# Kernel optimization log

Measured on AMD Instinct MI355X. Metric: run time of the kernel, lower is better.

Reference implementation:

```python
import jax, jax.numpy as jnp
from jax import lax
import numpy as np

H = 512  # hidden_size

def lstm_cell(x, h, c, w_ih, w_hh):
    # gates: [B, 4H], pytorch LSTMCell gate order i, f, g, o
    gates = x @ w_ih.T + h @ w_hh.T
    i, f, g, o = jnp.split(gates, 4, axis=-1)
    c_new = jax.nn.sigmoid(f) * c + jax.nn.sigmoid(i) * jnp.tanh(g)
    h_new = jax.nn.sigmoid(o) * jnp.tanh(c_new)
    return h_new, c_new

def run_layer(xs, w_ih, w_hh):
    # xs: [T, B, D] -> hs, cs: [T, B, H]
    B = xs.shape[1]
    h0 = jnp.zeros((B, H), xs.dtype)
    c0 = jnp.zeros((B, H), xs.dtype)
    def step(carry, x):
        h, c = carry
        h, c = lstm_cell(x, h, c, w_ih, w_hh)
        return (h, c), (h, c)
    _, (hs, cs) = lax.scan(step, (h0, c0), xs)
    return hs, cs

def stacked(x, weights, reverse):
    # Faithful to apex stackedRNN: for reverse pass, the returned hidden
    # (collect_hidden=False) is the state after the FIRST reversed step
    # (seq == seq_len-1), per the `elif seq == seq_len - 1` branch.
    xs = x[::-1] if reverse else x
    h_hid, c_hid = [], []
    cur = xs
    for w_ih, w_hh in weights:
        hs, cs = run_layer(cur, w_ih, w_hh)
        cur = hs
        idx = 0 if reverse else -1
        h_hid.append(hs[idx])
        c_hid.append(cs[idx])
    out = cur[::-1] if reverse else cur
    return out, jnp.stack(h_hid), jnp.stack(c_hid)

def setup_inputs() -> dict:
    key = jax.random.key(0)
    ks = jax.random.split(key, 9)
    T, B, D = 1024, 64, 512
    stdev = 1.0 / np.sqrt(H)
    d = {"x": jax.random.normal(ks[0], (T, B, D), dtype=jnp.float32)}
    names = ["w_ih_f0", "w_hh_f0", "w_ih_f1", "w_hh_f1",
             "w_ih_b0", "w_hh_b0", "w_ih_b1", "w_hh_b1"]
    for i, n in enumerate(names):
        d[n] = jax.random.uniform(ks[i + 1], (4 * H, 512), dtype=jnp.float32,
                                  minval=-stdev, maxval=stdev)
    return d

def reference(x, w_ih_f0, w_hh_f0, w_ih_f1, w_hh_f1,
              w_ih_b0, w_hh_b0, w_ih_b1, w_hh_b1):
    fwd_out, fh, fc = stacked(x, [(w_ih_f0, w_hh_f0), (w_ih_f1, w_hh_f1)], False)
    bwd_out, bh, bc = stacked(x, [(w_ih_b0, w_hh_b0), (w_ih_b1, w_hh_b1)], True)
    output = jnp.concatenate([fwd_out, bwd_out], axis=-1)  # [T, B, 2H]
    h = jnp.concatenate([fh, bh], axis=-1)  # [nLayers, B, 2H]
    c = jnp.concatenate([fc, bc], axis=-1)  # [nLayers, B, 2H]
    return output, h, c
```

## Files before the change

### kernel.cpp

```cpp
#include <hip/hip_runtime.h>

typedef short  sh8  __attribute__((ext_vector_type(8)));
typedef float  f32x4 __attribute__((ext_vector_type(4)));
typedef ushort ush4 __attribute__((ext_vector_type(4)));

#define TS 1024
#define BB 64
#define HH 512

#define HOFF 67108864ull
#define HC_DELTA 131072ull

#define BAR_WORDS 2120

static __device__ __forceinline__ float sigm(float x){ return 1.f/(1.f+__expf(-x)); }
static __device__ __forceinline__ float tanh_(float x){ return 1.f - 2.f/(__expf(2.f*x)+1.f); }
static __device__ __forceinline__ ushort f2bf(float f){
  unsigned u = __float_as_uint(f);
  u += 0x7fffu + ((u>>16)&1u);
  return (ushort)(u>>16);
}

__global__ __launch_bounds__(256) void cvt_w(
    const float* __restrict__ p0, const float* __restrict__ p1,
    const float* __restrict__ p2, const float* __restrict__ p3,
    const float* __restrict__ p4, const float* __restrict__ p5,
    const float* __restrict__ p6, const float* __restrict__ p7,
    ushort* __restrict__ wb, unsigned* __restrict__ bar)
{
  if (blockIdx.x == 0){
    for (unsigned i = threadIdx.x; i < BAR_WORDS; i += 256) bar[i] = 0u;
  }
  const unsigned gid = blockIdx.x*256 + threadIdx.x;
  const unsigned m = gid >> 18;
  const unsigned o = gid & 0x3FFFFu;
  const float* src;
  switch(m){
    case 0: src=p0; break; case 1: src=p1; break; case 2: src=p2; break; case 3: src=p3; break;
    case 4: src=p4; break; case 5: src=p5; break; case 6: src=p6; break; default: src=p7; break;
  }
  float4 f = *(const float4*)(src + (size_t)o*4);
  ush4 r; r.x=f2bf(f.x); r.y=f2bf(f.y); r.z=f2bf(f.z); r.w=f2bf(f.w);
  *(ush4*)(wb + ((size_t)m<<20) + (size_t)o*4) = r;
}

__global__ __launch_bounds__(256) void cvt_x(
    const float* __restrict__ x, ushort* __restrict__ xb)
{
  const unsigned gid = blockIdx.x*256 + threadIdx.x;
  float4 f = *(const float4*)(x + (size_t)gid*4);
  ush4 r; r.x=f2bf(f.x); r.y=f2bf(f.y); r.z=f2bf(f.z); r.w=f2bf(f.w);
  *(ush4*)(xb + (size_t)gid*4) = r;
}

static __device__ __forceinline__ sh8 ld_cvt8(const float* p){
  float4 f0 = *(const float4*)p;
  float4 f1 = *(const float4*)(p+4);
  sh8 r;
  r[0]=(short)f2bf(f0.x); r[1]=(short)f2bf(f0.y); r[2]=(short)f2bf(f0.z); r[3]=(short)f2bf(f0.w);
  r[4]=(short)f2bf(f1.x); r[5]=(short)f2bf(f1.y); r[6]=(short)f2bf(f1.z); r[7]=(short)f2bf(f1.w);
  return r;
}

static __device__ __forceinline__ void pipe_barrier(unsigned* ctr, unsigned* abortf)
{
  __syncthreads();
  if (threadIdx.x == 0){
    if (__hip_atomic_load(abortf, __ATOMIC_RELAXED, __HIP_MEMORY_SCOPE_AGENT) == 0u){
      __hip_atomic_fetch_add(ctr, 1u, __ATOMIC_RELEASE, __HIP_MEMORY_SCOPE_AGENT);
      unsigned spins = 0;
      while (__hip_atomic_load(ctr, __ATOMIC_ACQUIRE, __HIP_MEMORY_SCOPE_AGENT) < 128u){
        __builtin_amdgcn_s_sleep(1);
        if (++spins > (1u<<22)){
          __hip_atomic_store(abortf, 1u, __ATOMIC_RELAXED, __HIP_MEMORY_SCOPE_AGENT);
          break;
        }
      }
    }
  }
  __syncthreads();
}

template<bool XBF>
__global__ __launch_bounds__(256, 1) void lstm_persist(
    const float* __restrict__ xf, const ushort* __restrict__ xb,
    const ushort* __restrict__ wb,
    float* __restrict__ out, ushort* __restrict__ h_ws, unsigned* __restrict__ bar)
{
  const int group = blockIdx.x >> 6;
  const int w     = blockIdx.x & 63;
  const int lane  = threadIdx.x & 63;
  const int wv    = threadIdx.x >> 6;
  const int n     = lane & 15;
  const int q     = lane >> 4;

  unsigned* ctrbase = bar + (size_t)(group & 1) * 1056;
  unsigned* abortf  = bar + 2112;

  int wbase;
  if      (group==0) wbase = 0;
  else if (group==1) wbase = 4;
  else if (group==2) wbase = 2;
  else               wbase = 6;
  const ushort* wih = wb + ((size_t)wbase<<20);
  const ushort* whh = wb + ((size_t)(wbase+1)<<20);

  const int r0 = ((n>>3)  )*512 + w*8 + (n&7);
  const int r1 = ((n>>3)+2)*512 + w*8 + (n&7);
  const int arow = wv*16 + n;
  const size_t aoff  = (size_t)arow*HH + q*8;
  const size_t b0off = (size_t)r0*HH + q*8;
  const size_t b1off = (size_t)r1*HH + q*8;

  sh8 wi0[16], wi1[16], wh0[16], wh1[16];
#pragma unroll
  for (int kk=0; kk<16; ++kk){
    wi0[kk] = *(const sh8*)(wih + b0off + (size_t)kk*32);
    wi1[kk] = *(const sh8*)(wih + b1off + (size_t)kk*32);
    wh0[kk] = *(const sh8*)(whh + b0off + (size_t)kk*32);
    wh1[kk] = *(const sh8*)(whh + b1off + (size_t)kk*32);
  }

  const bool low = (n < 8);
  const int  col = w*8 + (n&7);
  float c_reg[4] = {0.f,0.f,0.f,0.f};

  sh8 ax[16];
  if (group < 2){
    if constexpr (XBF){
      const ushort* p = xb + ((group==0) ? (size_t)0 : (size_t)(TS-1)*(BB*HH));
#pragma unroll
      for (int kk=0;kk<16;++kk) ax[kk] = *(const sh8*)(p + aoff + (size_t)kk*32);
    } else {
      const float* p = xf + ((group==0) ? (size_t)0 : (size_t)(TS-1)*(BB*HH));
#pragma unroll
      for (int kk=0;kk<16;++kk) ax[kk] = ld_cvt8(p + aoff + (size_t)kk*32);
    }
  }

  for (int s = 0; s <= TS; ++s){
    const bool active = (group < 2) ? (s < TS) : (s > 0);
    if (active){
      const int  step   = (group < 2) ? s : (s-1);
      const bool have_h = (step > 0);
      const ushort* hsrc = h_ws + ((size_t)group*2 + ((s-1)&1))*(BB*HH);

      if (group >= 2){
        const ushort* xsb = h_ws + ((size_t)(group-2)*2 + ((s-1)&1))*(BB*HH);
#pragma unroll
        for (int kk=0;kk<16;++kk) ax[kk] = *(const sh8*)(xsb + aoff + (size_t)kk*32);
      }

      f32x4 acc0 = {0.f,0.f,0.f,0.f};
      f32x4 acc1 = {0.f,0.f,0.f,0.f};
#pragma unroll
      for (int kk=0;kk<16;++kk){
        acc0 = __builtin_amdgcn_mfma_f32_16x16x32_bf16(ax[kk], wi0[kk], acc0, 0, 0, 0);
        acc1 = __builtin_amdgcn_mfma_f32_16x16x32_bf16(ax[kk], wi1[kk], acc1, 0, 0, 0);
      }
      if (have_h){
#pragma unroll
        for (int kk=0;kk<16;++kk){
          sh8 ah = *(const sh8*)(hsrc + aoff + (size_t)kk*32);
          acc0 = __builtin_amdgcn_mfma_f32_16x16x32_bf16(ah, wh0[kk], acc0, 0, 0, 0);
          acc1 = __builtin_amdgcn_mfma_f32_16x16x32_bf16(ah, wh1[kk], acc1, 0, 0, 0);
        }
      }

      ushort* hdst = h_ws + ((size_t)group*2 + (s&1))*(BB*HH);
#pragma unroll
      for (int r=0; r<4; ++r){
        float v0 = acc0[r], v1 = acc1[r];
        float p0 = __shfl_xor(v0, 8, 64);
        float p1 = __shfl_xor(v1, 8, 64);
        if (low){
          const int row = wv*16 + q*4 + r;
          const float iv=v0, fv=p0, gv=v1, ov=p1;
          float cn = sigm(fv)*c_reg[r] + sigm(iv)*tanh_(gv);
          float hn = sigm(ov)*tanh_(cn);
          c_reg[r] = cn;
          hdst[(size_t)row*HH + col] = f2bf(hn);

          if (group == 2){
            out[((size_t)(s-1)*BB + row)*1024 + col] = hn;
          } else if (group == 3){
            out[((size_t)(TS-s)*BB + row)*1024 + 512 + col] = hn;
          }

          bool cap = false; size_t hoff = 0;
          if      (group==0 && s==TS-1){ cap=true; hoff = HOFF + (size_t)row*1024 + col; }
          else if (group==1 && s==0)   { cap=true; hoff = HOFF + (size_t)row*1024 + 512 + col; }
          else if (group==2 && s==TS)  { cap=true; hoff = HOFF + (size_t)(BB+row)*1024 + col; }
          else if (group==3 && s==1)   { cap=true; hoff = HOFF + (size_t)(BB+row)*1024 + 512 + col; }
          if (cap){
            out[hoff] = hn;
            out[hoff + HC_DELTA] = cn;
          }
        }
      }
    }

    if (group < 2 && (s+1) < TS){
      if constexpr (XBF){
        const ushort* p = xb + ((group==0) ? (size_t)(s+1)*(BB*HH) : (size_t)(TS-2-s)*(BB*HH));
#pragma unroll
        for (int kk=0;kk<16;++kk) ax[kk] = *(const sh8*)(p + aoff + (size_t)kk*32);
      } else {
        const float* p = xf + ((group==0) ? (size_t)(s+1)*(BB*HH) : (size_t)(TS-2-s)*(BB*HH));
#pragma unroll
        for (int kk=0;kk<16;++kk) ax[kk] = ld_cvt8(p + aoff + (size_t)kk*32);
      }
    }

    if (s < TS) pipe_barrier(ctrbase + s, abortf);
  }
}

extern "C" void kernel_launch(void* const* d_in, const int* in_sizes, int n_in,
                              void* d_out, int out_size, void* d_ws, size_t ws_size,
                              hipStream_t stream)
{
  const float* x = (const float*)d_in[0];
  const float* W[8];
  for (int i = 0; i < 8; ++i) W[i] = (const float*)d_in[i+1];
  float* out = (float*)d_out;

  char* ws = (char*)d_ws;
  unsigned* bar  = (unsigned*)ws;
  ushort*   h_ws = (ushort*)(ws + 524288);
  ushort*   wb   = (ushort*)(ws + 1048576);
  ushort*   xb   = (ushort*)(ws + 1048576 + 16777216);
  const bool xbf = ws_size >= (1048576ull + 16777216ull + 67108864ull);

  cvt_w<<<dim3(8192), dim3(256), 0, stream>>>(W[0],W[1],W[2],W[3],W[4],W[5],W[6],W[7], wb, bar);
  if (xbf) cvt_x<<<dim3(32768), dim3(256), 0, stream>>>(x, xb);

  if (xbf)
    lstm_persist<true ><<<dim3(256), dim3(256), 0, stream>>>(x, xb, wb, out, h_ws, bar);
  else
    lstm_persist<false><<<dim3(256), dim3(256), 0, stream>>>(x, xb, wb, out, h_ws, bar);
}
```

Baseline: 17.44 ms.

## Use relaxed agent-scope atomics for hidden-state exchange and stream weights from memory

The grid barrier switches from release/acquire to relaxed atomics. Hidden-state loads and stores become relaxed agent-scope atomics, so the acquire-driven cache invalidation and writeback on every step should no longer be needed. Weight fragments are no longer pinned in registers and are reloaded from global memory each step, which frees a large share of the VGPRs. Recurrent h inputs are now prefetched into registers before the MFMA loop, and adjacent bf16 h outputs are packed into 32-bit stores. The trade-off is extra per-step weight traffic through the caches and weaker memory ordering that leans on the compiler barriers and atomic visibility; the spin-timeout limit is also lowered.

```diff
diff --git a/kernel.cpp b/kernel.cpp
--- a/kernel.cpp
+++ b/kernel.cpp
@@ -19,6 +19,16 @@
   unsigned u = __float_as_uint(f);
   u += 0x7fffu + ((u>>16)&1u);
   return (ushort)(u>>16);
+}
+
+static __device__ __forceinline__ sh8 ldh8(const ushort* p){
+  union { unsigned long long u[2]; sh8 v; } r;
+  r.u[0] = __hip_atomic_load((const unsigned long long*)p,     __ATOMIC_RELAXED, __HIP_MEMORY_SCOPE_AGENT);
+  r.u[1] = __hip_atomic_load((const unsigned long long*)(p+4), __ATOMIC_RELAXED, __HIP_MEMORY_SCOPE_AGENT);
+  return r.v;
+}
+static __device__ __forceinline__ void sth4(ushort* p, unsigned v){
+  __hip_atomic_store((unsigned*)p, v, __ATOMIC_RELAXED, __HIP_MEMORY_SCOPE_AGENT);
 }
 
 __global__ __launch_bounds__(256) void cvt_w(
@@ -65,19 +75,21 @@
 static __device__ __forceinline__ void pipe_barrier(unsigned* ctr, unsigned* abortf)
 {
   __syncthreads();
+  asm volatile("" ::: "memory");
   if (threadIdx.x == 0){
     if (__hip_atomic_load(abortf, __ATOMIC_RELAXED, __HIP_MEMORY_SCOPE_AGENT) == 0u){
-      __hip_atomic_fetch_add(ctr, 1u, __ATOMIC_RELEASE, __HIP_MEMORY_SCOPE_AGENT);
+      __hip_atomic_fetch_add(ctr, 1u, __ATOMIC_RELAXED, __HIP_MEMORY_SCOPE_AGENT);
       unsigned spins = 0;
-      while (__hip_atomic_load(ctr, __ATOMIC_ACQUIRE, __HIP_MEMORY_SCOPE_AGENT) < 128u){
+      while (__hip_atomic_load(ctr, __ATOMIC_RELAXED, __HIP_MEMORY_SCOPE_AGENT) < 128u){
         __builtin_amdgcn_s_sleep(1);
-        if (++spins > (1u<<22)){
+        if (++spins > (1u<<19)){
           __hip_atomic_store(abortf, 1u, __ATOMIC_RELAXED, __HIP_MEMORY_SCOPE_AGENT);
           break;
         }
       }
     }
   }
+  asm volatile("" ::: "memory");
   __syncthreads();
 }
 
@@ -112,15 +124,6 @@
   const size_t b0off = (size_t)r0*HH + q*8;
   const size_t b1off = (size_t)r1*HH + q*8;
 
-  sh8 wi0[16], wi1[16], wh0[16], wh1[16];
-#pragma unroll
-  for (int kk=0; kk<16; ++kk){
-    wi0[kk] = *(const sh8*)(wih + b0off + (size_t)kk*32);
-    wi1[kk] = *(const sh8*)(wih + b1off + (size_t)kk*32);
-    wh0[kk] = *(const sh8*)(whh + b0off + (size_t)kk*32);
-    wh1[kk] = *(const sh8*)(whh + b1off + (size_t)kk*32);
-  }
-
   const bool low = (n < 8);
   const int  col = w*8 + (n&7);
   float c_reg[4] = {0.f,0.f,0.f,0.f};
@@ -148,22 +151,27 @@
       if (group >= 2){
         const ushort* xsb = h_ws + ((size_t)(group-2)*2 + ((s-1)&1))*(BB*HH);
 #pragma unroll
-        for (int kk=0;kk<16;++kk) ax[kk] = *(const sh8*)(xsb + aoff + (size_t)kk*32);
+        for (int kk=0;kk<16;++kk) ax[kk] = ldh8(xsb + aoff + (size_t)kk*32);
+      }
+
+      sh8 ah[16];
+      if (have_h){
+#pragma unroll
+        for (int kk=0;kk<16;++kk) ah[kk] = ldh8(hsrc + aoff + (size_t)kk*32);
       }
 
       f32x4 acc0 = {0.f,0.f,0.f,0.f};
       f32x4 acc1 = {0.f,0.f,0.f,0.f};
 #pragma unroll
       for (int kk=0;kk<16;++kk){
-        acc0 = __builtin_amdgcn_mfma_f32_16x16x32_bf16(ax[kk], wi0[kk], acc0, 0, 0, 0);
-        acc1 = __builtin_amdgcn_mfma_f32_16x16x32_bf16(ax[kk], wi1[kk], acc1, 0, 0, 0);
+        acc0 = __builtin_amdgcn_mfma_f32_16x16x32_bf16(ax[kk], *(const sh8*)(wih + b0off + (size_t)kk*32), acc0, 0, 0, 0);
+        acc1 = __builtin_amdgcn_mfma_f32_16x16x32_bf16(ax[kk], *(const sh8*)(wih + b1off + (size_t)kk*32), acc1, 0, 0, 0);
       }
       if (have_h){
 #pragma unroll
         for (int kk=0;kk<16;++kk){
-          sh8 ah = *(const sh8*)(hsrc + aoff + (size_t)kk*32);
-          acc0 = __builtin_amdgcn_mfma_f32_16x16x32_bf16(ah, wh0[kk], acc0, 0, 0, 0);
-          acc1 = __builtin_amdgcn_mfma_f32_16x16x32_bf16(ah, wh1[kk], acc1, 0, 0, 0);
+          acc0 = __builtin_amdgcn_mfma_f32_16x16x32_bf16(ah[kk], *(const sh8*)(whh + b0off + (size_t)kk*32), acc0, 0, 0, 0);
+          acc1 = __builtin_amdgcn_mfma_f32_16x16x32_bf16(ah[kk], *(const sh8*)(whh + b1off + (size_t)kk*32), acc1, 0, 0, 0);
         }
       }
 
@@ -179,7 +187,11 @@
           float cn = sigm(fv)*c_reg[r] + sigm(iv)*tanh_(gv);
           float hn = sigm(ov)*tanh_(cn);
           c_reg[r] = cn;
-          hdst[(size_t)row*HH + col] = f2bf(hn);
+
+          unsigned hb = (unsigned)f2bf(hn);
+          unsigned ob = (unsigned)__shfl_xor((int)hb, 1, 64);
+          if (!(n & 1))
+            sth4(hdst + (size_t)row*HH + col, hb | (ob << 16));
 
           if (group == 2){
             out[((size_t)(s-1)*BB + row)*1024 + col] = hn;
```

Measured after the change: 20.29 ms. 16.3% more time.
